# Kernel optimization log

Measured on AMD Instinct MI355X. Metric: run time of the kernel, lower is better.

Reference implementation:

```python
import jax, jax.numpy as jnp
import numpy as np

LN_EPS = 1e-5

def setup_inputs() -> dict:
    key = jax.random.key(0)
    k1, k2, k3, k4 = jax.random.split(key, 4)
    B, N, D, E = 2, 50000, 128, 800000
    H = jax.random.normal(k1, (B, N, D), dtype=jnp.float32)
    src = jax.random.randint(k2, (E,), 0, N, dtype=jnp.int64)
    dst = jax.random.randint(k3, (E,), 0, N, dtype=jnp.int64)
    W = jax.random.normal(k4, (D, D), dtype=jnp.float32) * (1.0 / np.sqrt(D))
    gamma = jnp.ones((D,), dtype=jnp.float32)
    beta = jnp.zeros((D,), dtype=jnp.float32)
    return {"H": H, "src": src, "dst": dst, "W": W, "gamma": gamma, "beta": beta}

def reference(H, src, dst, W, gamma, beta):
    # m = Linear(H) (no bias): [B,N,D]
    m = jnp.einsum('bnd,de->bne', H, W)
    # gather messages at src, scatter-add into dst along node dim
    agg = jnp.zeros_like(m).at[:, dst, :].add(m[:, src, :])
    x = H + jax.nn.gelu(agg, approximate=False)
    # LayerNorm over last dim
    mu = jnp.mean(x, axis=-1, keepdims=True)
    var = jnp.var(x, axis=-1, keepdims=True)
    return (x - mu) * jax.lax.rsqrt(var + LN_EPS) * gamma + beta
```

## Files before the change

kernel.cpp:

```cpp
#include <hip/hip_runtime.h>
#include <math.h>

#define DIM 128
#define LN_EPS 1e-5f
#define CAP 64
#define EPT 8

typedef unsigned short bf16_t;
typedef unsigned short u16;
typedef __attribute__((ext_vector_type(8))) short bf16x8;
typedef __attribute__((ext_vector_type(4))) float f32x4;

__device__ __forceinline__ bf16_t f2bf(float f) {
    unsigned u = __builtin_bit_cast(unsigned, f);
    u += 0x7FFFu + ((u >> 16) & 1u);
    return (bf16_t)(u >> 16);
}
__device__ __forceinline__ float bf2f(bf16_t h) {
    unsigned u = ((unsigned)h) << 16;
    return __builtin_bit_cast(float, u);
}

__global__ __launch_bounds__(256) void prep_kernel(
    const float* __restrict__ W, bf16_t* __restrict__ WT,
    int* __restrict__ cursor, int N)
{
    if (blockIdx.x < 16) {
        int i = blockIdx.x * 256 + threadIdx.x;
        float4 w = ((const float4*)W)[i];
        int k  = i >> 5;
        int n0 = (i & 31) * 4;
        WT[(n0 + 0) * DIM + k] = f2bf(w.x);
        WT[(n0 + 1) * DIM + k] = f2bf(w.y);
        WT[(n0 + 2) * DIM + k] = f2bf(w.z);
        WT[(n0 + 3) * DIM + k] = f2bf(w.w);
    } else {
        int i = (blockIdx.x - 16) * 256 + threadIdx.x;
        if (i < N) cursor[i] = 0;
    }
}

__global__ __launch_bounds__(256) void gemm_fill_kernel(
    const float* __restrict__ Hmat, const bf16_t* __restrict__ WT,
    bf16_t* __restrict__ Mout,
    const int* __restrict__ src, const int* __restrict__ dst,
    int* __restrict__ cursor, u16* __restrict__ eidxT,
    int nrows, int N, int E, int FB)
{
    if ((int)blockIdx.x < FB) {
        const int base = blockIdx.x * (256 * EPT) + threadIdx.x;
        int d[EPT], s[EPT];
        #pragma unroll
        for (int i = 0; i < EPT; ++i) {
            int e = base + i * 256;
            bool ok = (e < E);
            d[i] = ok ? dst[e] : -1;
            s[i] = ok ? src[e] : 0;
        }
        #pragma unroll
        for (int i = 0; i < EPT; ++i) {
            if (d[i] >= 0) {
                int pos = atomicAdd(&cursor[d[i]], 1);
                if (pos < CAP) eidxT[(size_t)pos * N + d[i]] = (u16)s[i];
            }
        }
        return;
    }

    const int tid = threadIdx.x;
    const int gblock = blockIdx.x - FB;
    const int wave = tid >> 6;
    const int lane = tid & 63;
    const int quad = lane >> 4;
    const int l15  = lane & 15;

    const int arow = gblock * 64 + wave * 16 + l15;
    const float* Arow = Hmat + (size_t)((arow < nrows) ? arow : 0) * DIM;

    f32x4 acc[8];
    #pragma unroll
    for (int t = 0; t < 8; ++t) acc[t] = (f32x4){0.f, 0.f, 0.f, 0.f};

    #pragma unroll
    for (int ks = 0; ks < 4; ++ks) {
        const int k0 = ks * 32 + quad * 8;
        float4 a0 = *(const float4*)&Arow[k0];
        float4 a1 = *(const float4*)&Arow[k0 + 4];
        bf16x8 af;
        af[0] = (short)f2bf(a0.x); af[1] = (short)f2bf(a0.y);
        af[2] = (short)f2bf(a0.z); af[3] = (short)f2bf(a0.w);
        af[4] = (short)f2bf(a1.x); af[5] = (short)f2bf(a1.y);
        af[6] = (short)f2bf(a1.z); af[7] = (short)f2bf(a1.w);

        #pragma unroll
        for (int t = 0; t < 8; ++t) {
            bf16x8 bf = *(const bf16x8*)&WT[(t * 16 + l15) * DIM + k0];
            acc[t] = __builtin_amdgcn_mfma_f32_16x16x32_bf16(af, bf, acc[t], 0, 0, 0);
        }
    }

    const int outrowbase = gblock * 64 + wave * 16 + quad * 4;
    #pragma unroll
    for (int r = 0; r < 4; ++r) {
        int rr = outrowbase + r;
        if (rr < nrows) {
            int b = (rr >= N) ? 1 : 0;
            int n = rr - (b ? N : 0);
            bf16_t* orow = Mout + ((size_t)n * 2 + b) * DIM + l15;
            #pragma unroll
            for (int t = 0; t < 8; ++t)
                orow[t * 16] = f2bf(acc[t][r]);
        }
    }
}

__global__ __launch_bounds__(256) void gather_kernel(
    const bf16_t* __restrict__ M, const float* __restrict__ Hmat,
    const int* __restrict__ cursor, const u16* __restrict__ eidxT,
    const float* __restrict__ gamma, const float* __restrict__ beta,
    float* __restrict__ out, int N)
{
    const int wave = threadIdx.x >> 6;
    const int lane = threadIdx.x & 63;
    const int node = blockIdx.x * 4 + wave;
    if (node >= N) return;

    const int b  = lane >> 5;
    const int c4 = lane & 31;

    int cnt = cursor[node];
    if (cnt > CAP) cnt = CAP;

    int myidx = (lane < cnt) ? (int)eidxT[(size_t)lane * N + node] : 0;

    const ushort4* M4 = (const ushort4*)M;

    float acc0 = 0.f, acc1 = 0.f, acc2 = 0.f, acc3 = 0.f;
    int j = 0;
    for (; j + 8 <= cnt; j += 8) {
        ushort4 v[8];
        #pragma unroll
        for (int q = 0; q < 8; ++q) {
            int s = __shfl(myidx, j + q, 64);
            v[q] = M4[(size_t)s * 64 + lane];
        }
        #pragma unroll
        for (int q = 0; q < 8; ++q) {
            acc0 += bf2f(v[q].x); acc1 += bf2f(v[q].y);
            acc2 += bf2f(v[q].z); acc3 += bf2f(v[q].w);
        }
    }
    for (; j < cnt; ++j) {
        int s = __shfl(myidx, j, 64);
        ushort4 v0 = M4[(size_t)s * 64 + lane];
        acc0 += bf2f(v0.x); acc1 += bf2f(v0.y);
        acc2 += bf2f(v0.z); acc3 += bf2f(v0.w);
    }

    const size_t elembase = ((size_t)b * N + node) * DIM + c4 * 4;
    float4 h = *(const float4*)&Hmat[elembase];
    const float inv_sqrt2 = 0.70710678118654752f;
    float x0 = h.x + 0.5f * acc0 * (1.f + erff(acc0 * inv_sqrt2));
    float x1 = h.y + 0.5f * acc1 * (1.f + erff(acc1 * inv_sqrt2));
    float x2 = h.z + 0.5f * acc2 * (1.f + erff(acc2 * inv_sqrt2));
    float x3 = h.w + 0.5f * acc3 * (1.f + erff(acc3 * inv_sqrt2));

    float s  = x0 + x1 + x2 + x3;
    float ss = x0 * x0 + x1 * x1 + x2 * x2 + x3 * x3;
    #pragma unroll
    for (int o = 16; o > 0; o >>= 1) {
        s  += __shfl_xor(s,  o, 64);
        ss += __shfl_xor(ss, o, 64);
    }
    const float mean = s * (1.f / DIM);
    const float var  = ss * (1.f / DIM) - mean * mean;
    const float inv  = rsqrtf(var + LN_EPS);

    float4 gm = *(const float4*)&gamma[c4 * 4];
    float4 bt = *(const float4*)&beta[c4 * 4];
    float4 o;
    o.x = (x0 - mean) * inv * gm.x + bt.x;
    o.y = (x1 - mean) * inv * gm.y + bt.y;
    o.z = (x2 - mean) * inv * gm.z + bt.z;
    o.w = (x3 - mean) * inv * gm.w + bt.w;
    *(float4*)&out[elembase] = o;
}

extern "C" void kernel_launch(void* const* d_in, const int* in_sizes, int n_in,
                              void* d_out, int out_size, void* d_ws, size_t ws_size,
                              hipStream_t stream)
{
    const float* H     = (const float*)d_in[0];
    const int*   src   = (const int*)  d_in[1];
    const int*   dst   = (const int*)  d_in[2];
    const float* W     = (const float*)d_in[3];
    const float* gamma = (const float*)d_in[4];
    const float* beta  = (const float*)d_in[5];
    float* out = (float*)d_out;

    const int E     = in_sizes[1];
    const int total = in_sizes[0];
    const int nrows = total / DIM;
    const int N     = nrows / 2;

    char* ws = (char*)d_ws;
    bf16_t* Mbuf = (bf16_t*)ws;   ws += (size_t)total * sizeof(bf16_t);
    int* cursor  = (int*)ws;      ws += (size_t)N * sizeof(int);
    u16* eidxT   = (u16*)ws;      ws += (size_t)CAP * N * sizeof(u16);
    bf16_t* WT   = (bf16_t*)ws;   ws += (size_t)DIM * DIM * sizeof(bf16_t);

    prep_kernel<<<16 + (N + 255) / 256, 256, 0, stream>>>(W, WT, cursor, N);

    const int FB = (E + 256 * EPT - 1) / (256 * EPT);
    const int GB = (nrows + 63) / 64;

    gemm_fill_kernel<<<FB + GB, 256, 0, stream>>>(H, WT, Mbuf, src, dst,
                                                  cursor, eidxT, nrows, N, E, FB);

    gather_kernel<<<(N + 3) / 4, 256, 0, stream>>>(Mbuf, H, cursor, eidxT,
                                                   gamma, beta, out, N);
}
```

Baseline: 227.6 us.

## Aggregate raw features before the linear layer and fuse GEMM with GELU/LayerNorm

Uses linearity to swap the order: H is first converted to bf16 in node-interleaved layout, neighbours are gathered and summed, and only then is the sum multiplied by W. The GEMM is fused with GELU, residual add and LayerNorm through a shared-memory staging tile, which removes the separate read of H in the gather pass. The cost is an extra bf16 round trip for the aggregated buffer, a bf16 rounding of the summed aggregate before the matmul (a change in numerics), and an H conversion pass. The cursor reset moves to hipMemsetAsync.

After: 260.6 us. 1.14x slower.

```diff
diff --git a/kernel.cpp b/kernel.cpp
--- a/kernel.cpp
+++ b/kernel.cpp
@@ -20,13 +20,42 @@
     unsigned u = ((unsigned)h) << 16;
     return __builtin_bit_cast(float, u);
 }
-
-__global__ __launch_bounds__(256) void prep_kernel(
-    const float* __restrict__ W, bf16_t* __restrict__ WT,
-    int* __restrict__ cursor, int N)
-{
-    if (blockIdx.x < 16) {
-        int i = blockIdx.x * 256 + threadIdx.x;
+__device__ __forceinline__ float gelu(float v) {
+    const float inv_sqrt2 = 0.70710678118654752f;
+    return 0.5f * v * (1.f + erff(v * inv_sqrt2));
+}
+
+__global__ __launch_bounds__(256) void prep_fill_kernel(
+    const float* __restrict__ Hmat, const float* __restrict__ W,
+    const int* __restrict__ src, const int* __restrict__ dst,
+    int* __restrict__ cursor, u16* __restrict__ eidxT,
+    bf16_t* __restrict__ WT, bf16_t* __restrict__ Hb,
+    int nrows, int N, int E, int FB)
+{
+    const int bx = (int)blockIdx.x;
+    const int tid = threadIdx.x;
+
+    if (bx < FB) {
+        const int base = bx * (256 * EPT) + tid;
+        int d[EPT], s[EPT];
+        #pragma unroll
+        for (int i = 0; i < EPT; ++i) {
+            int e = base + i * 256;
+            bool ok = (e < E);
+            d[i] = ok ? dst[e] : -1;
+            s[i] = ok ? src[e] : 0;
+        }
+        #pragma unroll
+        for (int i = 0; i < EPT; ++i) {
+            if (d[i] >= 0) {
+                int pos = atomicAdd(&cursor[d[i]], 1);
+                if (pos < CAP) eidxT[(size_t)pos * N + d[i]] = (u16)s[i];
+            }
+        }
+        return;
+    }
+    if (bx < FB + 16) {
+        int i = (bx - FB) * 256 + tid;
         float4 w = ((const float4*)W)[i];
         int k  = i >> 5;
         int n0 = (i & 31) * 4;
@@ -34,48 +63,85 @@
         WT[(n0 + 1) * DIM + k] = f2bf(w.y);
         WT[(n0 + 2) * DIM + k] = f2bf(w.z);
         WT[(n0 + 3) * DIM + k] = f2bf(w.w);
-    } else {
-        int i = (blockIdx.x - 16) * 256 + threadIdx.x;
-        if (i < N) cursor[i] = 0;
-    }
-}
-
-__global__ __launch_bounds__(256) void gemm_fill_kernel(
-    const float* __restrict__ Hmat, const bf16_t* __restrict__ WT,
-    bf16_t* __restrict__ Mout,
-    const int* __restrict__ src, const int* __restrict__ dst,
-    int* __restrict__ cursor, u16* __restrict__ eidxT,
-    int nrows, int N, int E, int FB)
-{
-    if ((int)blockIdx.x < FB) {
-        const int base = blockIdx.x * (256 * EPT) + threadIdx.x;
-        int d[EPT], s[EPT];
-        #pragma unroll
-        for (int i = 0; i < EPT; ++i) {
-            int e = base + i * 256;
-            bool ok = (e < E);
-            d[i] = ok ? dst[e] : -1;
-            s[i] = ok ? src[e] : 0;
-        }
-        #pragma unroll
-        for (int i = 0; i < EPT; ++i) {
-            if (d[i] >= 0) {
-                int pos = atomicAdd(&cursor[d[i]], 1);
-                if (pos < CAP) eidxT[(size_t)pos * N + d[i]] = (u16)s[i];
-            }
-        }
         return;
     }
-
-    const int tid = threadIdx.x;
-    const int gblock = blockIdx.x - FB;
+    int i = (bx - FB - 16) * 256 + tid;
+    if (i < nrows * (DIM / 4)) {
+        int row = i >> 5;
+        int c4  = i & 31;
+        int b   = (row >= N) ? 1 : 0;
+        int n   = row - (b ? N : 0);
+        float4 h = ((const float4*)Hmat)[i];
+        ushort4 o;
+        o.x = f2bf(h.x); o.y = f2bf(h.y); o.z = f2bf(h.z); o.w = f2bf(h.w);
+        ((ushort4*)Hb)[((size_t)n * 2 + b) * 32 + c4] = o;
+    }
+}
+
+__global__ __launch_bounds__(256) void gather_sum_kernel(
+    const bf16_t* __restrict__ Hb, const int* __restrict__ cursor,
+    const u16* __restrict__ eidxT, bf16_t* __restrict__ Agg, int N)
+{
+    const int wave = threadIdx.x >> 6;
+    const int lane = threadIdx.x & 63;
+    const int node = blockIdx.x * 4 + wave;
+    if (node >= N) return;
+
+    const int b  = lane >> 5;
+    const int c4 = lane & 31;
+
+    int cnt = cursor[node];
+    if (cnt > CAP) cnt = CAP;
+
+    int myidx = (lane < cnt) ? (int)eidxT[(size_t)lane * N + node] : 0;
+
+    const ushort4* H4 = (const ushort4*)Hb;
+
+    float acc0 = 0.f, acc1 = 0.f, acc2 = 0.f, acc3 = 0.f;
+    int j = 0;
+    for (; j + 8 <= cnt; j += 8) {
+        ushort4 v[8];
+        #pragma unroll
+        for (int q = 0; q < 8; ++q) {
+            int s = __shfl(myidx, j + q, 64);
+            v[q] = H4[(size_t)s * 64 + lane];
+        }
+        #pragma unroll
+        for (int q = 0; q < 8; ++q) {
+            acc0 += bf2f(v[q].x); acc1 += bf2f(v[q].y);
+            acc2 += bf2f(v[q].z); acc3 += bf2f(v[q].w);
+        }
+    }
+    for (; j < cnt; ++j) {
+        int s = __shfl(myidx, j, 64);
+        ushort4 v0 = H4[(size_t)s * 64 + lane];
+        acc0 += bf2f(v0.x); acc1 += bf2f(v0.y);
+        acc2 += bf2f(v0.z); acc3 += bf2f(v0.w);
+    }
+
+    ushort4 o;
+    o.x = f2bf(acc0); o.y = f2bf(acc1); o.z = f2bf(acc2); o.w = f2bf(acc3);
+    ((ushort4*)Agg)[((size_t)b * N + node) * 32 + c4] = o;
+}
+
+#define CPAD 132
+__global__ __launch_bounds__(256) void gemm_ln_kernel(
+    const bf16_t* __restrict__ Agg, const bf16_t* __restrict__ WT,
+    const float* __restrict__ Hmat,
+    const float* __restrict__ gamma, const float* __restrict__ beta,
+    float* __restrict__ out, int nrows)
+{
+    __shared__ float sC[4][16 * CPAD];
+
+    const int tid  = threadIdx.x;
     const int wave = tid >> 6;
     const int lane = tid & 63;
     const int quad = lane >> 4;
     const int l15  = lane & 15;
 
-    const int arow = gblock * 64 + wave * 16 + l15;
-    const float* Arow = Hmat + (size_t)((arow < nrows) ? arow : 0) * DIM;
+    int arow = blockIdx.x * 64 + wave * 16 + l15;
+    if (arow >= nrows) arow = nrows - 1;
+    const bf16_t* Arow = Agg + (size_t)arow * DIM;
 
     f32x4 acc[8];
     #pragma unroll
@@ -84,14 +150,7 @@
     #pragma unroll
     for (int ks = 0; ks < 4; ++ks) {
         const int k0 = ks * 32 + quad * 8;
-        float4 a0 = *(const float4*)&Arow[k0];
-        float4 a1 = *(const float4*)&Arow[k0 + 4];
-        bf16x8 af;
-        af[0] = (short)f2bf(a0.x); af[1] = (short)f2bf(a0.y);
-        af[2] = (short)f2bf(a0.z); af[3] = (short)f2bf(a0.w);
-        af[4] = (short)f2bf(a1.x); af[5] = (short)f2bf(a1.y);
-        af[6] = (short)f2bf(a1.z); af[7] = (short)f2bf(a1.w);
-
+        bf16x8 af = *(const bf16x8*)&Arow[k0];
         #pragma unroll
         for (int t = 0; t < 8; ++t) {
             bf16x8 bf = *(const bf16x8*)&WT[(t * 16 + l15) * DIM + k0];
@@ -99,91 +158,53 @@
         }
     }
 
-    const int outrowbase = gblock * 64 + wave * 16 + quad * 4;
-    #pragma unroll
-    for (int r = 0; r < 4; ++r) {
-        int rr = outrowbase + r;
-        if (rr < nrows) {
-            int b = (rr >= N) ? 1 : 0;
-            int n = rr - (b ? N : 0);
-            bf16_t* orow = Mout + ((size_t)n * 2 + b) * DIM + l15;
-            #pragma unroll
-            for (int t = 0; t < 8; ++t)
-                orow[t * 16] = f2bf(acc[t][r]);
-        }
-    }
-}
-
-__global__ __launch_bounds__(256) void gather_kernel(
-    const bf16_t* __restrict__ M, const float* __restrict__ Hmat,
-    const int* __restrict__ cursor, const u16* __restrict__ eidxT,
-    const float* __restrict__ gamma, const float* __restrict__ beta,
-    float* __restrict__ out, int N)
-{
-    const int wave = threadIdx.x >> 6;
-    const int lane = threadIdx.x & 63;
-    const int node = blockIdx.x * 4 + wave;
-    if (node >= N) return;
-
-    const int b  = lane >> 5;
-    const int c4 = lane & 31;
-
-    int cnt = cursor[node];
-    if (cnt > CAP) cnt = CAP;
-
-    int myidx = (lane < cnt) ? (int)eidxT[(size_t)lane * N + node] : 0;
-
-    const ushort4* M4 = (const ushort4*)M;
-
-    float acc0 = 0.f, acc1 = 0.f, acc2 = 0.f, acc3 = 0.f;
-    int j = 0;
-    for (; j + 8 <= cnt; j += 8) {
-        ushort4 v[8];
-        #pragma unroll
-        for (int q = 0; q < 8; ++q) {
-            int s = __shfl(myidx, j + q, 64);
-            v[q] = M4[(size_t)s * 64 + lane];
-        }
-        #pragma unroll
-        for (int q = 0; q < 8; ++q) {
-            acc0 += bf2f(v[q].x); acc1 += bf2f(v[q].y);
-            acc2 += bf2f(v[q].z); acc3 += bf2f(v[q].w);
-        }
-    }
-    for (; j < cnt; ++j) {
-        int s = __shfl(myidx, j, 64);
-        ushort4 v0 = M4[(size_t)s * 64 + lane];
-        acc0 += bf2f(v0.x); acc1 += bf2f(v0.y);
-        acc2 += bf2f(v0.z); acc3 += bf2f(v0.w);
-    }
-
-    const size_t elembase = ((size_t)b * N + node) * DIM + c4 * 4;
-    float4 h = *(const float4*)&Hmat[elembase];
-    const float inv_sqrt2 = 0.70710678118654752f;
-    float x0 = h.x + 0.5f * acc0 * (1.f + erff(acc0 * inv_sqrt2));
-    float x1 = h.y + 0.5f * acc1 * (1.f + erff(acc1 * inv_sqrt2));
-    float x2 = h.z + 0.5f * acc2 * (1.f + erff(acc2 * inv_sqrt2));
-    float x3 = h.w + 0.5f * acc3 * (1.f + erff(acc3 * inv_sqrt2));
-
-    float s  = x0 + x1 + x2 + x3;
-    float ss = x0 * x0 + x1 * x1 + x2 * x2 + x3 * x3;
-    #pragma unroll
-    for (int o = 16; o > 0; o >>= 1) {
-        s  += __shfl_xor(s,  o, 64);
-        ss += __shfl_xor(ss, o, 64);
-    }
+    #pragma unroll
+    for (int t = 0; t < 8; ++t)
+        #pragma unroll
+        for (int r = 0; r < 4; ++r)
+            sC[wave][(quad * 4 + r) * CPAD + t * 16 + l15] = acc[t][r];
+    __syncthreads();
+
+    const int row16 = lane & 15;
+    const int qtr   = lane >> 4;
+    const int grow  = blockIdx.x * 64 + wave * 16 + row16;
+    if (grow >= nrows) return;
+
+    const float* sRow = &sC[wave][row16 * CPAD + qtr * 32];
+    const float* hRow = &Hmat[(size_t)grow * DIM + qtr * 32];
+
+    float4 x[8];
+    float s = 0.f, ss = 0.f;
+    #pragma unroll
+    for (int j = 0; j < 8; ++j) {
+        float4 c = *(const float4*)&sRow[j * 4];
+        float4 h = *(const float4*)&hRow[j * 4];
+        float4 v;
+        v.x = h.x + gelu(c.x); v.y = h.y + gelu(c.y);
+        v.z = h.z + gelu(c.z); v.w = h.w + gelu(c.w);
+        x[j] = v;
+        s  += v.x + v.y + v.z + v.w;
+        ss += v.x * v.x + v.y * v.y + v.z * v.z + v.w * v.w;
+    }
+    s  += __shfl_xor(s, 16, 64);  ss += __shfl_xor(ss, 16, 64);
+    s  += __shfl_xor(s, 32, 64);  ss += __shfl_xor(ss, 32, 64);
+
     const float mean = s * (1.f / DIM);
     const float var  = ss * (1.f / DIM) - mean * mean;
     const float inv  = rsqrtf(var + LN_EPS);
 
-    float4 gm = *(const float4*)&gamma[c4 * 4];
-    float4 bt = *(const float4*)&beta[c4 * 4];
-    float4 o;
-    o.x = (x0 - mean) * inv * gm.x + bt.x;
-    o.y = (x1 - mean) * inv * gm.y + bt.y;
-    o.z = (x2 - mean) * inv * gm.z + bt.z;
-    o.w = (x3 - mean) * inv * gm.w + bt.w;
-    *(float4*)&out[elembase] = o;
+    float* oRow = &out[(size_t)grow * DIM + qtr * 32];
+    #pragma unroll
+    for (int j = 0; j < 8; ++j) {
+        float4 g = *(const float4*)&gamma[qtr * 32 + j * 4];
+        float4 bt = *(const float4*)&beta[qtr * 32 + j * 4];
+        float4 o;
+        o.x = (x[j].x - mean) * inv * g.x + bt.x;
+        o.y = (x[j].y - mean) * inv * g.y + bt.y;
+        o.z = (x[j].z - mean) * inv * g.z + bt.z;
+        o.w = (x[j].w - mean) * inv * g.w + bt.w;
+        *(float4*)&oRow[j * 4] = o;
+    }
 }
 
 extern "C" void kernel_launch(void* const* d_in, const int* in_sizes, int n_in,
@@ -204,19 +225,22 @@
     const int N     = nrows / 2;
 
     char* ws = (char*)d_ws;
-    bf16_t* Mbuf = (bf16_t*)ws;   ws += (size_t)total * sizeof(bf16_t);
+    bf16_t* Hb   = (bf16_t*)ws;   ws += (size_t)total * sizeof(bf16_t);
+    bf16_t* Agg  = (bf16_t*)ws;   ws += (size_t)total * sizeof(bf16_t);
     int* cursor  = (int*)ws;      ws += (size_t)N * sizeof(int);
     u16* eidxT   = (u16*)ws;      ws += (size_t)CAP * N * sizeof(u16);
     bf16_t* WT   = (bf16_t*)ws;   ws += (size_t)DIM * DIM * sizeof(bf16_t);
 
-    prep_kernel<<<16 + (N + 255) / 256, 256, 0, stream>>>(W, WT, cursor, N);
+    hipMemsetAsync(cursor, 0, (size_t)N * sizeof(int), stream);
 
     const int FB = (E + 256 * EPT - 1) / (256 * EPT);
-    const int GB = (nrows + 63) / 64;
-
-    gemm_fill_kernel<<<FB + GB, 256, 0, stream>>>(H, WT, Mbuf, src, dst,
-                                                  cursor, eidxT, nrows, N, E, FB);
-
-    gather_kernel<<<(N + 3) / 4, 256, 0, stream>>>(Mbuf, H, cursor, eidxT,
-                                                   gamma, beta, out, N);
-}
+    const int HB = (nrows * (DIM / 4) + 255) / 256;
+
+    prep_fill_kernel<<<FB + 16 + HB, 256, 0, stream>>>(
+        H, W, src, dst, cursor, eidxT, WT, Hb, nrows, N, E, FB);
+
+    gather_sum_kernel<<<(N + 3) / 4, 256, 0, stream>>>(Hb, cursor, eidxT, Agg, N);
+
+    gemm_ln_kernel<<<(nrows + 63) / 64, 256, 0, stream>>>(
+        Agg, WT, H, gamma, beta, out, nrows);
+}
```
